# Kernel tuning notes

Hardware: AMD Instinct MI355X
Metric: run time of the kernel (lower is better)

The kernel has to match this reference:

```python
import jax, jax.numpy as jnp
import numpy as np

EPS = 1e-6
NUM_HEADS = 16
ROPE_THETA = 100000.0


def _rope_tables(seq_len, head_dim, theta):
    inv_freq = 1.0 / (theta ** (np.arange(0, head_dim, 2, dtype=np.float32) / head_dim))
    t = np.arange(seq_len, dtype=np.float32)
    freqs = np.outer(t, inv_freq)                      # (S, head_dim//2)
    emb = np.concatenate([freqs, freqs], axis=-1)      # (S, head_dim)
    return jnp.asarray(np.cos(emb))[None], jnp.asarray(np.sin(emb))[None]  # (1,S,D)


def setup_inputs() -> dict:
    key = jax.random.key(0)
    ks = jax.random.split(key, 6)
    B, S, H = 2, 2048, 1024
    head_dim = H // NUM_HEADS
    cos, sin = _rope_tables(S, head_dim, ROPE_THETA)
    scale = 0.02
    return {
        "hidden_states": jax.random.normal(ks[0], (B, S, H), dtype=jnp.float32),
        "cos": cos, "sin": sin,
        "Wq": jax.random.normal(ks[1], (H, H), dtype=jnp.float32) * scale,
        "bq": jnp.zeros((H,), dtype=jnp.float32),
        "Wk": jax.random.normal(ks[2], (H, H), dtype=jnp.float32) * scale,
        "bk": jnp.zeros((H,), dtype=jnp.float32),
        "Wv": jax.random.normal(ks[3], (H, H), dtype=jnp.float32) * scale,
        "bv": jnp.zeros((H,), dtype=jnp.float32),
        "Wo": jax.random.normal(ks[4], (H, H), dtype=jnp.float32) * scale,
        "bo": jnp.zeros((H,), dtype=jnp.float32),
        "rms_weight": jnp.ones((H,), dtype=jnp.float32),
    }


def _rms_norm(x, w):
    var = jnp.mean(x * x, axis=-1, keepdims=True)
    return x * jax.lax.rsqrt(var + EPS) * w


def _rotate_half(x):
    x1, x2 = jnp.split(x, 2, axis=-1)
    return jnp.concatenate([-x2, x1], axis=-1)


def reference(hidden_states, cos, sin, Wq, bq, Wk, bk, Wv, bv, Wo, bo, rms_weight):
    B, S, H = hidden_states.shape
    D = H // NUM_HEADS
    q = hidden_states @ Wq.T + bq
    k = hidden_states @ Wk.T + bk
    v = hidden_states @ Wv.T + bv
    # RMSNorm over full hidden dim BEFORE head split (as in original)
    q = _rms_norm(q, rms_weight)
    k = _rms_norm(k, rms_weight)
    # (B,S,H) -> (B,heads,S,D)
    q = q.reshape(B, S, NUM_HEADS, D).transpose(0, 2, 1, 3)
    k = k.reshape(B, S, NUM_HEADS, D).transpose(0, 2, 1, 3)
    v = v.reshape(B, S, NUM_HEADS, D).transpose(0, 2, 1, 3)
    # RoPE: cos/sin (1,S,D) -> unsqueeze head dim
    c = cos[:, None, :, :]
    s = sin[:, None, :, :]
    q = q * c + _rotate_half(q) * s
    k = k * c + _rotate_half(k) * s
    # attention (faithful: boolean tril mask is ADDED as 0/1, not -inf)
    scale = D ** 0.5
    scores = jnp.einsum("bhqd,bhkd->bhqk", q, k) / scale
    mask = jnp.tril(jnp.ones((S, S), dtype=scores.dtype))  # +1 on causal, +0 elsewhere
    attn = jax.nn.softmax(scores + mask, axis=-1)
    out = jnp.einsum("bhqk,bhkd->bhqd", attn, v)
    out = out.transpose(0, 2, 1, 3).reshape(B, S, H)
    return out @ Wo.T + bo
```

## Files before the change

kernel.cpp:

```cpp
#include <hip/hip_runtime.h>

typedef unsigned short u16;
typedef __attribute__((ext_vector_type(8))) _Float16 half8;
typedef __attribute__((ext_vector_type(2))) __fp16 fp16x2;
typedef __attribute__((ext_vector_type(4))) float f32x4;
typedef __attribute__((ext_vector_type(16))) float f32x16;

#define MFMAH(A,B,C) __builtin_amdgcn_mfma_f32_16x16x32_f16(A,B,C,0,0,0)
#define MFMA32(A,B,C) __builtin_amdgcn_mfma_f32_32x32x16_f16(A,B,C,0,0,0)
#define LOG2E 1.4426950408889634f
#define C1 0.18033688011112042f

__device__ __forceinline__ u16 f2h(float f){
  _Float16 h = (_Float16)f; u16 r; __builtin_memcpy(&r,&h,2); return r;
}
__device__ __forceinline__ float h2f(u16 v){
  _Float16 h; __builtin_memcpy(&h,&v,2); return (float)h;
}
__device__ __forceinline__ unsigned int pack_h2(float a, float b){
  fp16x2 h = __builtin_amdgcn_cvt_pkrtz(a,b);
  unsigned int r; __builtin_memcpy(&r,&h,4); return r;
}

__device__ __forceinline__ void async_ld16(const void* g, void* l) {
  __builtin_amdgcn_global_load_lds(
      (const __attribute__((address_space(1))) unsigned int*)g,
      (__attribute__((address_space(3))) unsigned int*)l, 16, 0, 0);
}

__global__ __launch_bounds__(256) void cast_all(const float* __restrict__ hs,
    const float* __restrict__ wq, const float* __restrict__ wk,
    const float* __restrict__ wv, const float* __restrict__ wo,
    u16* __restrict__ dst)
{
  unsigned int i = blockIdx.x*256 + threadIdx.x;
  size_t el = (size_t)i * 8;
  const float* src; size_t off;
  if (el < 4194304) { src = hs; off = el; }
  else {
    unsigned int r = (unsigned int)((el - 4194304) >> 20);
    src = (r==0)?wq:(r==1)?wk:(r==2)?wv:wo;
    off = (el - 4194304) & 1048575;
  }
  float4 a = *reinterpret_cast<const float4*>(src+off);
  float4 b = *reinterpret_cast<const float4*>(src+off+4);
  uint4 o = {pack_h2(a.x,a.y), pack_h2(a.z,a.w), pack_h2(b.x,b.y), pack_h2(b.z,b.w)};
  *reinterpret_cast<uint4*>(dst + el) = o;
}

__global__ __launch_bounds__(256) void gemm_qkv(const u16* __restrict__ A,
                                                const u16* __restrict__ W,
                                                const float* __restrict__ bqp,
                                                const float* __restrict__ bkp,
                                                const float* __restrict__ bvp,
                                                u16* __restrict__ qout,
                                                u16* __restrict__ kout,
                                                u16* __restrict__ vout,
                                                int M, int K)
{
  __shared__ __align__(16) u16 lds_a[128*32];
  __shared__ __align__(16) u16 lds_w[128*32];
  const int t = threadIdx.x;
  const int lane = t & 63, wave = t >> 6;
  const int wm = wave >> 1, wn = wave & 1;
  const int lr = lane & 15, quad = lane >> 4;
  const int n0 = blockIdx.x * 128, m0 = blockIdx.y * 128;
  const int wbase = t & 192;
  const int which = n0 >> 10;

  const f32x4 fzero = {0.f,0.f,0.f,0.f};
  f32x4 acc[4][4];
  #pragma unroll
  for (int i=0;i<4;++i)
    #pragma unroll
    for (int j=0;j<4;++j) acc[i][j] = fzero;

  if (which < 2) {
    for (int k0 = 0; k0 < K; k0 += 32) {
      __syncthreads();
      #pragma unroll
      for (int it=0; it<2; ++it) {
        int idx = it*256 + t;
        int row = idx >> 2, c8 = (idx & 3) * 8;
        int lbase = (it*256 + wbase) * 8;
        async_ld16(&A[(size_t)(m0+row)*K + k0 + c8], &lds_a[lbase]);
        async_ld16(&W[(size_t)(n0+row)*K + k0 + c8], &lds_w[lbase]);
      }
      __syncthreads();
      half8 af[4], bfr[4];
      #pragma unroll
      for (int mt=0; mt<4; ++mt)
        af[mt] = *reinterpret_cast<const half8*>(&lds_a[(wm*64 + mt*16 + lr)*32 + quad*8]);
      #pragma unroll
      for (int nt=0; nt<4; ++nt)
        bfr[nt] = *reinterpret_cast<const half8*>(&lds_w[(wn*64 + nt*16 + lr)*32 + quad*8]);
      #pragma unroll
      for (int mt=0; mt<4; ++mt)
        #pragma unroll
        for (int nt=0; nt<4; ++nt)
          acc[mt][nt] = MFMAH(bfr[nt], af[mt], acc[mt][nt]);
    }
    const float* bp = which ? bkp : bqp;
    u16* dst = which ? kout : qout;
    #pragma unroll
    for (int nt=0; nt<4; ++nt) {
      int nn = (n0 & 1023) + wn*64 + nt*16 + quad*4;
      float4 bv = *reinterpret_cast<const float4*>(&bp[nn]);
      int hh = nn >> 6, d4 = nn & 63;
      #pragma unroll
      for (int mt=0; mt<4; ++mt) {
        int m = m0 + wm*64 + mt*16 + lr;
        int b = m >> 11, s = m & 2047;
        uint2 o = {pack_h2(acc[mt][nt][0]+bv.x, acc[mt][nt][1]+bv.y),
                   pack_h2(acc[mt][nt][2]+bv.z, acc[mt][nt][3]+bv.w)};
        *reinterpret_cast<uint2*>(&dst[((size_t)(b*16 + hh)*2048 + s)*64 + d4]) = o;
      }
    }
  } else {
    for (int k0 = 0; k0 < K; k0 += 32) {
      __syncthreads();
      #pragma unroll
      for (int it=0; it<2; ++it) {
        int idx = it*256 + t;
        int row = idx >> 2, c8 = (idx & 3) * 8;
        int lbase = (it*256 + wbase) * 8;
        async_ld16(&A[(size_t)(m0+row)*K + k0 + c8], &lds_a[lbase]);
        async_ld16(&W[(size_t)(n0+row)*K + k0 + c8], &lds_w[lbase]);
      }
      __syncthreads();
      half8 af[4], bfr[4];
      #pragma unroll
      for (int mt=0; mt<4; ++mt)
        af[mt] = *reinterpret_cast<const half8*>(&lds_a[(wm*64 + mt*16 + lr)*32 + quad*8]);
      #pragma unroll
      for (int nt=0; nt<4; ++nt)
        bfr[nt] = *reinterpret_cast<const half8*>(&lds_w[(wn*64 + nt*16 + lr)*32 + quad*8]);
      #pragma unroll
      for (int mt=0; mt<4; ++mt)
        #pragma unroll
        for (int nt=0; nt<4; ++nt)
          acc[mt][nt] = MFMAH(af[mt], bfr[nt], acc[mt][nt]);
    }
    #pragma unroll
    for (int nt=0; nt<4; ++nt) {
      int nn = (n0 & 1023) + wn*64 + nt*16 + lr;
      float bv = bvp[nn];
      int hh = nn >> 6, d = nn & 63;
      #pragma unroll
      for (int mt=0; mt<4; ++mt) {
        int m = m0 + wm*64 + mt*16 + quad*4;
        int b = m >> 11, s = m & 2047;
        uint2 o = {pack_h2(acc[mt][nt][0]+bv, acc[mt][nt][1]+bv),
                   pack_h2(acc[mt][nt][2]+bv, acc[mt][nt][3]+bv)};
        *reinterpret_cast<uint2*>(&vout[((size_t)(b*16 + hh)*64 + d)*2048 + s]) = o;
      }
    }
  }
}

__global__ __launch_bounds__(256) void gemm_o(const u16* __restrict__ A,
                                              const u16* __restrict__ W,
                                              const float* __restrict__ bias,
                                              float* __restrict__ O,
                                              int M, int N, int K)
{
  __shared__ __align__(16) u16 lds_a[128*32];
  __shared__ __align__(16) u16 lds_w[64*32];
  const int t = threadIdx.x;
  const int lane = t & 63, wm = t >> 6;
  const int lr = lane & 15, quad = lane >> 4;
  const int n0 = blockIdx.x * 64, m0 = blockIdx.y * 128;
  const int wbase = t & 192;

  const f32x4 fzero = {0.f,0.f,0.f,0.f};
  f32x4 acc[2][4];
  #pragma unroll
  for (int i=0;i<2;++i)
    #pragma unroll
    for (int j=0;j<4;++j) acc[i][j] = fzero;

  for (int k0 = 0; k0 < K; k0 += 32) {
    __syncthreads();
    #pragma unroll
    for (int it=0; it<2; ++it) {
      int idx = it*256 + t;
      int row = idx >> 2, c8 = (idx & 3) * 8;
      int lbase = (it*256 + wbase) * 8;
      async_ld16(&A[(size_t)(m0+row)*K + k0 + c8], &lds_a[lbase]);
    }
    async_ld16(&W[(size_t)(n0 + (t>>2))*K + k0 + (t&3)*8], &lds_w[wbase*8]);
    __syncthreads();
    half8 af[2], bfr[4];
    #pragma unroll
    for (int mt=0; mt<2; ++mt)
      af[mt] = *reinterpret_cast<const half8*>(&lds_a[(wm*32 + mt*16 + lr)*32 + quad*8]);
    #pragma unroll
    for (int nt=0; nt<4; ++nt)
      bfr[nt] = *reinterpret_cast<const half8*>(&lds_w[(nt*16 + lr)*32 + quad*8]);
    #pragma unroll
    for (int mt=0; mt<2; ++mt)
      #pragma unroll
      for (int nt=0; nt<4; ++nt)
        acc[mt][nt] = MFMAH(bfr[nt], af[mt], acc[mt][nt]);
  }

  #pragma unroll
  for (int nt=0; nt<4; ++nt) {
    int nb = n0 + nt*16 + quad*4;
    float4 bv = *reinterpret_cast<const float4*>(&bias[nb]);
    #pragma unroll
    for (int mt=0; mt<2; ++mt) {
      int m = m0 + wm*32 + mt*16 + lr;
      float4 o = {acc[mt][nt][0]+bv.x, acc[mt][nt][1]+bv.y,
                  acc[mt][nt][2]+bv.z, acc[mt][nt][3]+bv.w};
      *reinterpret_cast<float4*>(&O[(size_t)m * N + nb]) = o;
    }
  }
}

__global__ __launch_bounds__(128) void rmsrope(u16* __restrict__ qb, u16* __restrict__ kb,
                                               const float* __restrict__ cosb,
                                               const float* __restrict__ sinb,
                                               const float* __restrict__ w)
{
  u16* buf = blockIdx.y ? kb : qb;
  const int bs = blockIdx.x;
  const int b = bs >> 11, s = bs & 2047;
  const int t = threadIdx.x;
  const int h = t >> 3, d0 = (t & 7) * 4;
  size_t base = ((size_t)(b*16+h)*2048 + s)*64;

  uint2 u1 = *reinterpret_cast<const uint2*>(&buf[base + d0]);
  uint2 u2 = *reinterpret_cast<const uint2*>(&buf[base + d0 + 32]);
  u16 a1[4], a2[4];
  __builtin_memcpy(a1, &u1, 8); __builtin_memcpy(a2, &u2, 8);
  float x1[4], x2[4];
  float ss = 0.f;
  #pragma unroll
  for (int j=0;j<4;++j){
    x1[j] = h2f(a1[j]); x2[j] = h2f(a2[j]);
    ss += x1[j]*x1[j] + x2[j]*x2[j];
  }
  #pragma unroll
  for (int off=32; off>0; off>>=1) ss += __shfl_xor(ss, off, 64);
  __shared__ float red[2];
  if ((t & 63) == 0) red[t>>6] = ss;
  __syncthreads();
  float tot = red[0] + red[1];
  float r = rsqrtf(tot * (1.0f/1024.0f) + 1e-6f);

  float4 w1 = *reinterpret_cast<const float4*>(&w[h*64+d0]);
  float4 w2 = *reinterpret_cast<const float4*>(&w[h*64+d0+32]);
  float4 c1 = *reinterpret_cast<const float4*>(&cosb[s*64+d0]);
  float4 s1 = *reinterpret_cast<const float4*>(&sinb[s*64+d0]);
  float4 c2 = *reinterpret_cast<const float4*>(&cosb[s*64+d0+32]);
  float4 s2 = *reinterpret_cast<const float4*>(&sinb[s*64+d0+32]);
  float n1[4] = {x1[0]*r*w1.x, x1[1]*r*w1.y, x1[2]*r*w1.z, x1[3]*r*w1.w};
  float n2[4] = {x2[0]*r*w2.x, x2[1]*r*w2.y, x2[2]*r*w2.z, x2[3]*r*w2.w};
  float o1[4] = {n1[0]*c1.x - n2[0]*s1.x, n1[1]*c1.y - n2[1]*s1.y,
                 n1[2]*c1.z - n2[2]*s1.z, n1[3]*c1.w - n2[3]*s1.w};
  float o2[4] = {n2[0]*c2.x + n1[0]*s2.x, n2[1]*c2.y + n1[1]*s2.y,
                 n2[2]*c2.z + n1[2]*s2.z, n2[3]*c2.w + n1[3]*s2.w};
  uint2 v1 = {pack_h2(o1[0],o1[1]), pack_h2(o1[2],o1[3])};
  uint2 v2 = {pack_h2(o2[0],o2[1]), pack_h2(o2[2],o2[3])};
  *reinterpret_cast<uint2*>(&buf[base + d0])      = v1;
  *reinterpret_cast<uint2*>(&buf[base + d0 + 32]) = v2;
}

__global__ __launch_bounds__(256) void attn(const u16* __restrict__ qh,
                                            const u16* __restrict__ kh,
                                            const u16* __restrict__ vt,
                                            u16* __restrict__ ao)
{
  __shared__ __align__(16) u16 kbuf[2][64*72];
  __shared__ __align__(16) u16 vbuf[2][64*72];
  const int t = threadIdx.x;
  const int lane = t & 63, w = t >> 6;
  const int ql = lane & 31, hf = lane >> 5;
  const int qbase = blockIdx.x * 128;
  const int bh = blockIdx.y;
  const int b = bh >> 4, h = bh & 15;
  const size_t hb = (size_t)bh * 2048 * 64;
  const u16* qp = qh + hb;
  const u16* kp = kh + hb;
  const u16* vtp = vt + hb;

  const int q_abs = qbase + w*32 + ql;
  half8 qf[4];
  #pragma unroll
  for (int s=0;s<4;++s)
    qf[s] = *reinterpret_cast<const half8*>(&qp[(size_t)q_abs*64 + s*16 + hf*8]);

  const int row = t >> 3;
  const int cc = t & 7;
  const int base2 = 32*(cc>>2) + 16*((cc>>1)&1) + 4*(cc&1);
  const int kofs = row*72 + cc*8;
  const u16* kg = kp + (size_t)row*64 + cc*8;
  const u16* vg = vtp + (size_t)row*2048 + base2;

  const f32x16 fz16 = {0.f,0.f,0.f,0.f,0.f,0.f,0.f,0.f,0.f,0.f,0.f,0.f,0.f,0.f,0.f,0.f};
  f32x16 oacc[2];
  oacc[0] = fz16; oacc[1] = fz16;
  float lsum = 0.f;
  const int diag = (qbase + w*32) >> 6;

  {
    uint4 k0v = *reinterpret_cast<const uint4*>(kg);
    uint4 k1v = *reinterpret_cast<const uint4*>(kg + 32*64);
    uint2 a0 = *reinterpret_cast<const uint2*>(vg);
    uint2 a1 = *reinterpret_cast<const uint2*>(vg + 8);
    uint2 b0 = *reinterpret_cast<const uint2*>(vg + (size_t)32*2048);
    uint2 b1 = *reinterpret_cast<const uint2*>(vg + (size_t)32*2048 + 8);
    *reinterpret_cast<uint4*>(&kbuf[0][kofs])        = k0v;
    *reinterpret_cast<uint4*>(&kbuf[0][kofs+32*72])  = k1v;
    uint4 v0 = {a0.x,a0.y,a1.x,a1.y};
    uint4 v1 = {b0.x,b0.y,b1.x,b1.y};
    *reinterpret_cast<uint4*>(&vbuf[0][kofs])        = v0;
    *reinterpret_cast<uint4*>(&vbuf[0][kofs+32*72])  = v1;
  }

  for (int kt=0; kt<32; ++kt) {
    uint4 k0n, k1n; uint2 a0n, a1n, b0n, b1n;
    if (kt < 31) {
      const u16* kgn = kg + (size_t)(kt+1)*4096;
      const u16* vgn = vg + (kt+1)*64;
      k0n = *reinterpret_cast<const uint4*>(kgn);
      k1n = *reinterpret_cast<const uint4*>(kgn + 32*64);
      a0n = *reinterpret_cast<const uint2*>(vgn);
      a1n = *reinterpret_cast<const uint2*>(vgn + 8);
      b0n = *reinterpret_cast<const uint2*>(vgn + (size_t)32*2048);
      b1n = *reinterpret_cast<const uint2*>(vgn + (size_t)32*2048 + 8);
    }
    __syncthreads();
    const u16* kb = kbuf[kt & 1];
    const u16* vb = vbuf[kt & 1];

    unsigned int pk[4][4];
    #pragma unroll
    for (int kh2=0; kh2<2; ++kh2) {
      f32x16 z = fz16;
      #pragma unroll
      for (int s=0;s<4;++s) {
        half8 kf;
        __builtin_memcpy(&kf, &kb[(kh2*32+ql)*72 + s*16 + hf*8], 16);
        z = MFMA32(kf, qf[s], z);
      }
      float p[16];
      if (kt != diag) {
        float ml = (kt < diag) ? LOG2E : 0.0f;
        #pragma unroll
        for (int r=0;r<16;++r) {
          p[r] = __builtin_amdgcn_exp2f(__builtin_fmaf(z[r], C1, ml));
          lsum += p[r];
        }
      } else {
        #pragma unroll
        for (int r=0;r<16;++r) {
          int key = kt*64 + kh2*32 + (r&3) + 8*(r>>2) + 4*hf;
          float ml = (key <= q_abs) ? LOG2E : 0.0f;
          p[r] = __builtin_amdgcn_exp2f(__builtin_fmaf(z[r], C1, ml));
          lsum += p[r];
        }
      }
      #pragma unroll
      for (int t2=0;t2<2;++t2)
        #pragma unroll
        for (int jj=0;jj<4;++jj)
          pk[kh2*2+t2][jj] = pack_h2(p[t2*8+jj*2], p[t2*8+jj*2+1]);
    }

    #pragma unroll
    for (int st=0;st<4;++st) {
      uint4 pq = {pk[st][0], pk[st][1], pk[st][2], pk[st][3]};
      half8 pf; __builtin_memcpy(&pf, &pq, 16);
      #pragma unroll
      for (int dh=0; dh<2; ++dh) {
        half8 vf;
        __builtin_memcpy(&vf, &vb[(dh*32+ql)*72 + st*16 + hf*8], 16);
        oacc[dh] = MFMA32(vf, pf, oacc[dh]);
      }
    }

    if (kt < 31) {
      u16* kwn = &kbuf[(kt+1)&1][kofs];
      u16* vwn = &vbuf[(kt+1)&1][kofs];
      *reinterpret_cast<uint4*>(kwn)         = k0n;
      *reinterpret_cast<uint4*>(kwn + 32*72) = k1n;
      uint4 v0 = {a0n.x,a0n.y,a1n.x,a1n.y};
      uint4 v1 = {b0n.x,b0n.y,b1n.x,b1n.y};
      *reinterpret_cast<uint4*>(vwn)         = v0;
      *reinterpret_cast<uint4*>(vwn + 32*72) = v1;
    }
  }

  lsum += __shfl_xor(lsum, 32, 64);
  float inv = 1.0f / lsum;
  size_t rowbase = ((size_t)(b*2048 + q_abs))*1024 + h*64;
  #pragma unroll
  for (int dh=0; dh<2; ++dh)
    #pragma unroll
    for (int rq=0; rq<4; ++rq) {
      int dd = dh*32 + 8*rq + 4*hf;
      uint2 o = {pack_h2(oacc[dh][rq*4+0]*inv, oacc[dh][rq*4+1]*inv),
                 pack_h2(oacc[dh][rq*4+2]*inv, oacc[dh][rq*4+3]*inv)};
      *reinterpret_cast<uint2*>(&ao[rowbase + dd]) = o;
    }
}

extern "C" void kernel_launch(void* const* d_in, const int* in_sizes, int n_in,
                              void* d_out, int out_size, void* d_ws, size_t ws_size,
                              hipStream_t stream)
{
  const float* hs   = (const float*)d_in[0];
  const float* cosb = (const float*)d_in[1];
  const float* sinb = (const float*)d_in[2];
  const float* Wq   = (const float*)d_in[3];
  const float* bq   = (const float*)d_in[4];
  const float* Wk   = (const float*)d_in[5];
  const float* bk   = (const float*)d_in[6];
  const float* Wv   = (const float*)d_in[7];
  const float* bv   = (const float*)d_in[8];
  const float* Wo   = (const float*)d_in[9];
  const float* bo   = (const float*)d_in[10];
  const float* rw   = (const float*)d_in[11];

  const size_t NEL = (size_t)4096 * 1024;
  const size_t WEL = (size_t)1024 * 1024;
  u16* hsb = (u16*)d_ws;
  u16* wqb = hsb + NEL;
  u16* wob = wqb + 3*WEL;
  u16* qhb = wob + WEL;
  u16* khb = qhb + NEL;
  u16* vtb = khb + NEL;
  u16* aob = hsb;

  cast_all<<<4096, 256, 0, stream>>>(hs, Wq, Wk, Wv, Wo, hsb);
  gemm_qkv<<<dim3(24,32), 256, 0, stream>>>(hsb, wqb, bq, bk, bv, qhb, khb, vtb, 4096, 1024);
  rmsrope<<<dim3(4096,2), 128, 0, stream>>>(qhb, khb, cosb, sinb, rw);
  attn<<<dim3(16,32), 256, 0, stream>>>(qhb, khb, vtb, aob);
  gemm_o<<<dim3(16,32), 256, 0, stream>>>(aob, wob, bo, (float*)d_out, 4096, 1024, 1024);
}
```

Before: 222.3 us.

## Remap block indices for XCD-local L2 reuse and compute row sums via MFMA

```diff
diff --git a/kernel.cpp b/kernel.cpp
--- a/kernel.cpp
+++ b/kernel.cpp
@@ -64,7 +64,11 @@
   const int lane = t & 63, wave = t >> 6;
   const int wm = wave >> 1, wn = wave & 1;
   const int lr = lane & 15, quad = lane >> 4;
-  const int n0 = blockIdx.x * 128, m0 = blockIdx.y * 128;
+  const int flat = blockIdx.x;
+  const int xcd = flat & 7, slot = flat >> 3;
+  const int ln = slot % 12, lm = slot / 12;
+  const int n0 = ((xcd & 1) * 12 + ln) * 128;
+  const int m0 = ((xcd >> 1) * 8 + lm) * 128;
   const int wbase = t & 192;
   const int which = n0 >> 10;
 
@@ -169,7 +173,10 @@
   const int t = threadIdx.x;
   const int lane = t & 63, wm = t >> 6;
   const int lr = lane & 15, quad = lane >> 4;
-  const int n0 = blockIdx.x * 64, m0 = blockIdx.y * 128;
+  const int flat = blockIdx.x;
+  const int xcd = flat & 7, slot = flat >> 3;
+  const int n0 = (slot & 15) * 64;
+  const int m0 = ((xcd << 2) + (slot >> 4)) * 128;
   const int wbase = t & 192;
 
   const f32x4 fzero = {0.f,0.f,0.f,0.f};
@@ -277,8 +284,10 @@
   const int t = threadIdx.x;
   const int lane = t & 63, w = t >> 6;
   const int ql = lane & 31, hf = lane >> 5;
-  const int qbase = blockIdx.x * 128;
-  const int bh = blockIdx.y;
+  const int flat = blockIdx.x;
+  const int xcd = flat & 7, slot = flat >> 3;
+  const int bh = xcd + ((slot >> 4) << 3);
+  const int qbase = (slot & 15) * 128;
   const int b = bh >> 4, h = bh & 15;
   const size_t hb = (size_t)bh * 2048 * 64;
   const u16* qp = qh + hb;
@@ -290,6 +299,10 @@
   #pragma unroll
   for (int s=0;s<4;++s)
     qf[s] = *reinterpret_cast<const half8*>(&qp[(size_t)q_abs*64 + s*16 + hf*8]);
+
+  half8 onesf;
+  #pragma unroll
+  for (int i=0;i<8;++i) onesf[i] = (_Float16)1.0f;
 
   const int row = t >> 3;
   const int cc = t & 7;
@@ -301,7 +314,7 @@
   const f32x16 fz16 = {0.f,0.f,0.f,0.f,0.f,0.f,0.f,0.f,0.f,0.f,0.f,0.f,0.f,0.f,0.f,0.f};
   f32x16 oacc[2];
   oacc[0] = fz16; oacc[1] = fz16;
-  float lsum = 0.f;
+  f32x16 lacc = fz16;
   const int diag = (qbase + w*32) >> 6;
 
   {
@@ -349,17 +362,14 @@
       if (kt != diag) {
         float ml = (kt < diag) ? LOG2E : 0.0f;
         #pragma unroll
-        for (int r=0;r<16;++r) {
+        for (int r=0;r<16;++r)
           p[r] = __builtin_amdgcn_exp2f(__builtin_fmaf(z[r], C1, ml));
-          lsum += p[r];
-        }
       } else {
         #pragma unroll
         for (int r=0;r<16;++r) {
           int key = kt*64 + kh2*32 + (r&3) + 8*(r>>2) + 4*hf;
           float ml = (key <= q_abs) ? LOG2E : 0.0f;
           p[r] = __builtin_amdgcn_exp2f(__builtin_fmaf(z[r], C1, ml));
-          lsum += p[r];
         }
       }
       #pragma unroll
@@ -373,6 +383,7 @@
     for (int st=0;st<4;++st) {
       uint4 pq = {pk[st][0], pk[st][1], pk[st][2], pk[st][3]};
       half8 pf; __builtin_memcpy(&pf, &pq, 16);
+      lacc = MFMA32(onesf, pf, lacc);
       #pragma unroll
       for (int dh=0; dh<2; ++dh) {
         half8 vf;
@@ -393,8 +404,7 @@
     }
   }
 
-  lsum += __shfl_xor(lsum, 32, 64);
-  float inv = 1.0f / lsum;
+  float inv = 1.0f / lacc[0];
   size_t rowbase = ((size_t)(b*2048 + q_abs))*1024 + h*64;
   #pragma unroll
   for (int dh=0; dh<2; ++dh)
@@ -435,8 +445,8 @@
   u16* aob = hsb;
 
   cast_all<<<4096, 256, 0, stream>>>(hs, Wq, Wk, Wv, Wo, hsb);
-  gemm_qkv<<<dim3(24,32), 256, 0, stream>>>(hsb, wqb, bq, bk, bv, qhb, khb, vtb, 4096, 1024);
+  gemm_qkv<<<768, 256, 0, stream>>>(hsb, wqb, bq, bk, bv, qhb, khb, vtb, 4096, 1024);
   rmsrope<<<dim3(4096,2), 128, 0, stream>>>(qhb, khb, cosb, sinb, rw);
-  attn<<<dim3(16,32), 256, 0, stream>>>(qhb, khb, vtb, aob);
-  gemm_o<<<dim3(16,32), 256, 0, stream>>>(aob, wob, bo, (float*)d_out, 4096, 1024, 1024);
-}
+  attn<<<512, 256, 0, stream>>>(qhb, khb, vtb, aob);
+  gemm_o<<<512, 256, 0, stream>>>(aob, wob, bo, (float*)d_out, 4096, 1024, 1024);
+}
```

Result: no change. 219.3 us (-1.3%).
